# Kernel tuning notes

Measured on AMD Instinct MI355X. Metric: run time of the kernel, lower is better.

## Reference

```python
import jax, jax.numpy as jnp
import numpy as np

INPUT_SCALE = 1.0
TABLE_SIZE = 32
D_EMBED = 64
N = 1_000_000


def setup_inputs() -> dict:
    key = jax.random.key(0)
    k1, k2 = jax.random.split(key)
    x = jax.random.normal(k1, (N, 3), dtype=jnp.float32)
    # learned table parameter: [E, D, H, W] (batch dim of 1 dropped)
    table = jax.random.normal(k2, (D_EMBED, TABLE_SIZE, TABLE_SIZE, TABLE_SIZE), dtype=jnp.float32) * 0.1
    return {"x": x, "table": table}


def _grid_sample_3d(table, grid):
    """F.grid_sample(table[None], grid[None,None,None]) with mode='bilinear',
    padding_mode='zeros', align_corners=False.
    table: [E, D, H, W]; grid: [n, 3] with (x->W, y->H, z->D) order.
    Returns [n, E]."""
    E, Dz, Hy, Wx = table.shape
    sizes_f = jnp.array([Wx, Hy, Dz], dtype=table.dtype)
    dims_i = jnp.array([Wx, Hy, Dz], dtype=jnp.int32)
    # align_corners=False: pix = ((coord + 1) * size - 1) / 2
    pix = ((grid + 1.0) * sizes_f - 1.0) * 0.5   # [n, 3]
    p0f = jnp.floor(pix)
    frac = pix - p0f                              # [n, 3]
    p0 = p0f.astype(jnp.int32)
    tab_flat = table.reshape(E, -1).T             # [D*H*W, E]
    out = jnp.zeros((grid.shape[0], E), dtype=table.dtype)
    for dz in (0, 1):
        for dy in (0, 1):
            for dx in (0, 1):
                off = jnp.array([dx, dy, dz], dtype=jnp.int32)
                idx = p0 + off                                        # [n, 3]
                inb = jnp.all((idx >= 0) & (idx < dims_i), axis=-1)   # zeros padding
                idxc = jnp.clip(idx, 0, dims_i - 1)
                lin = (idxc[:, 2] * Hy + idxc[:, 1]) * Wx + idxc[:, 0]
                vals = tab_flat[lin]                                  # [n, E]
                w = jnp.prod(jnp.where(off == 1, frac, 1.0 - frac), axis=-1)
                out = out + vals * (w * inb.astype(table.dtype))[:, None]
    return out


def reference(x, table):
    xc = jnp.clip(x * INPUT_SCALE, -1.0, 1.0)
    return _grid_sample_3d(table, xc)
```

## Files before the change

### kernel.cpp

```cpp
#include <hip/hip_runtime.h>


constexpr int TSZ = 32;
constexpr int S   = TSZ * TSZ * TSZ;
constexpr int EMB = 64;

__device__ __forceinline__ unsigned short f32_to_bf16_rne(float f) {
  unsigned int u = __float_as_uint(f);
  unsigned int lsb = (u >> 16) & 1u;
  u += 0x7FFFu + lsb;
  return (unsigned short)(u >> 16);
}

__global__ __launch_bounds__(256) void transpose_table_k(
    const float* __restrict__ tab, unsigned short* __restrict__ tabT) {
  __shared__ float tile[EMB][EMB + 1];
  const int s_base = blockIdx.x * 64;
  const int t  = threadIdx.x;
  const int c0 = t & 63;
  const int r0 = t >> 6;
#pragma unroll
  for (int i = 0; i < 16; ++i) {
    const int e = r0 + 4 * i;
    tile[e][c0] = tab[(size_t)e * S + (s_base + c0)];
  }
  __syncthreads();
#pragma unroll
  for (int i = 0; i < 16; ++i) {
    const int s = r0 + 4 * i;
    tabT[(size_t)(s_base + s) * EMB + c0] = f32_to_bf16_rne(tile[c0][s]);
  }
}

__global__ __launch_bounds__(256) void embed_k(
    const float* __restrict__ x, const uint2* __restrict__ tabT,
    float4* __restrict__ out, int n) {
  const int gid = blockIdx.x * 256 + threadIdx.x;
  const int pt  = gid >> 4;
  if (pt >= n) return;
  const int cg = gid & 15;

  const float gx = fminf(fmaxf(x[3 * pt + 0], -1.f), 1.f);
  const float gy = fminf(fmaxf(x[3 * pt + 1], -1.f), 1.f);
  const float gz = fminf(fmaxf(x[3 * pt + 2], -1.f), 1.f);
  const float px = ((gx + 1.f) * 32.f - 1.f) * 0.5f;
  const float py = ((gy + 1.f) * 32.f - 1.f) * 0.5f;
  const float pz = ((gz + 1.f) * 32.f - 1.f) * 0.5f;

  const float fxf = floorf(px), fyf = floorf(py), fzf = floorf(pz);
  const int ix0 = (int)fxf, iy0 = (int)fyf, iz0 = (int)fzf;
  const float fx = px - fxf, fy = py - fyf, fz = pz - fzf;
  const float wx[2] = {1.f - fx, fx};
  const float wy[2] = {1.f - fy, fy};
  const float wz[2] = {1.f - fz, fz};

  float4 acc = make_float4(0.f, 0.f, 0.f, 0.f);
#pragma unroll
  for (int dz = 0; dz < 2; ++dz) {
    const int  iz  = iz0 + dz;
    const bool bz  = (unsigned)iz < (unsigned)TSZ;
    const int  izc = min(max(iz, 0), TSZ - 1);
#pragma unroll
    for (int dy = 0; dy < 2; ++dy) {
      const int  iy  = iy0 + dy;
      const bool by  = (unsigned)iy < (unsigned)TSZ;
      const int  iyc = min(max(iy, 0), TSZ - 1);
#pragma unroll
      for (int dx = 0; dx < 2; ++dx) {
        const int  ix  = ix0 + dx;
        const bool bx  = (unsigned)ix < (unsigned)TSZ;
        const int  ixc = min(max(ix, 0), TSZ - 1);
        float w = wz[dz] * wy[dy] * wx[dx];
        w = (bx && by && bz) ? w : 0.f;
        const int lin = (izc * TSZ + iyc) * TSZ + ixc;
        const uint2 q = tabT[lin * 16 + cg];
        const float v0 = __uint_as_float(q.x << 16);
        const float v1 = __uint_as_float(q.x & 0xFFFF0000u);
        const float v2 = __uint_as_float(q.y << 16);
        const float v3 = __uint_as_float(q.y & 0xFFFF0000u);
        acc.x = fmaf(w, v0, acc.x);
        acc.y = fmaf(w, v1, acc.y);
        acc.z = fmaf(w, v2, acc.z);
        acc.w = fmaf(w, v3, acc.w);
      }
    }
  }
  out[(size_t)pt * (EMB / 4) + cg] = acc;
}

__global__ __launch_bounds__(256) void embed_fallback_k(
    const float* __restrict__ x, const float* __restrict__ tab,
    float* __restrict__ out, int n) {
  const int gid = blockIdx.x * 256 + threadIdx.x;
  const int pt  = gid >> 6;
  if (pt >= n) return;
  const int e = gid & 63;

  const float gx = fminf(fmaxf(x[3 * pt + 0], -1.f), 1.f);
  const float gy = fminf(fmaxf(x[3 * pt + 1], -1.f), 1.f);
  const float gz = fminf(fmaxf(x[3 * pt + 2], -1.f), 1.f);
  const float px = ((gx + 1.f) * 32.f - 1.f) * 0.5f;
  const float py = ((gy + 1.f) * 32.f - 1.f) * 0.5f;
  const float pz = ((gz + 1.f) * 32.f - 1.f) * 0.5f;

  const float fxf = floorf(px), fyf = floorf(py), fzf = floorf(pz);
  const int ix0 = (int)fxf, iy0 = (int)fyf, iz0 = (int)fzf;
  const float fx = px - fxf, fy = py - fyf, fz = pz - fzf;
  const float wx[2] = {1.f - fx, fx};
  const float wy[2] = {1.f - fy, fy};
  const float wz[2] = {1.f - fz, fz};

  float acc = 0.f;
#pragma unroll
  for (int dz = 0; dz < 2; ++dz) {
    const int  iz  = iz0 + dz;
    const bool bz  = (unsigned)iz < (unsigned)TSZ;
    const int  izc = min(max(iz, 0), TSZ - 1);
#pragma unroll
    for (int dy = 0; dy < 2; ++dy) {
      const int  iy  = iy0 + dy;
      const bool by  = (unsigned)iy < (unsigned)TSZ;
      const int  iyc = min(max(iy, 0), TSZ - 1);
#pragma unroll
      for (int dx = 0; dx < 2; ++dx) {
        const int  ix  = ix0 + dx;
        const bool bx  = (unsigned)ix < (unsigned)TSZ;
        const int  ixc = min(max(ix, 0), TSZ - 1);
        float w = wz[dz] * wy[dy] * wx[dx];
        w = (bx && by && bz) ? w : 0.f;
        const int lin = (izc * TSZ + iyc) * TSZ + ixc;
        acc = fmaf(w, tab[(size_t)e * S + lin], acc);
      }
    }
  }
  out[(size_t)pt * EMB + e] = acc;
}

extern "C" void kernel_launch(void* const* d_in, const int* in_sizes, int n_in,
                              void* d_out, int out_size, void* d_ws,
                              size_t ws_size, hipStream_t stream) {
  const float* x   = (const float*)d_in[0];
  const float* tab = (const float*)d_in[1];
  float*       out = (float*)d_out;
  const int n = in_sizes[0] / 3;

  const size_t need = (size_t)S * EMB * sizeof(unsigned short);
  if (ws_size >= need) {
    unsigned short* tabT = (unsigned short*)d_ws;
    transpose_table_k<<<S / 64, 256, 0, stream>>>(tab, tabT);
    const int total  = n * 16;
    const int blocks = (total + 255) / 256;
    embed_k<<<blocks, 256, 0, stream>>>(x, (const uint2*)tabT, (float4*)out, n);
  } else {
    const int total  = n * EMB;
    const int blocks = (total + 255) / 256;
    embed_fallback_k<<<blocks, 256, 0, stream>>>(x, tab, out, n);
  }
}
```

Measured before the change: 331.7 us.

## Widen embed gather to 16-byte loads, 8 channels per thread, nontemporal IO

Result: faster. 319.7 us (-3.6%).

```diff
diff --git a/kernel.cpp b/kernel.cpp
--- a/kernel.cpp
+++ b/kernel.cpp
@@ -4,6 +4,8 @@
 constexpr int TSZ = 32;
 constexpr int S   = TSZ * TSZ * TSZ;
 constexpr int EMB = 64;
+
+typedef float floatx4 __attribute__((ext_vector_type(4)));
 
 __device__ __forceinline__ unsigned short f32_to_bf16_rne(float f) {
   unsigned int u = __float_as_uint(f);
@@ -33,16 +35,16 @@
 }
 
 __global__ __launch_bounds__(256) void embed_k(
-    const float* __restrict__ x, const uint2* __restrict__ tabT,
-    float4* __restrict__ out, int n) {
+    const float* __restrict__ x, const uint4* __restrict__ tabT,
+    float* __restrict__ out, int n) {
   const int gid = blockIdx.x * 256 + threadIdx.x;
-  const int pt  = gid >> 4;
+  const int pt  = gid >> 3;
   if (pt >= n) return;
-  const int cg = gid & 15;
+  const int c8 = gid & 7;
 
-  const float gx = fminf(fmaxf(x[3 * pt + 0], -1.f), 1.f);
-  const float gy = fminf(fmaxf(x[3 * pt + 1], -1.f), 1.f);
-  const float gz = fminf(fmaxf(x[3 * pt + 2], -1.f), 1.f);
+  const float gx = fminf(fmaxf(__builtin_nontemporal_load(&x[3 * pt + 0]), -1.f), 1.f);
+  const float gy = fminf(fmaxf(__builtin_nontemporal_load(&x[3 * pt + 1]), -1.f), 1.f);
+  const float gz = fminf(fmaxf(__builtin_nontemporal_load(&x[3 * pt + 2]), -1.f), 1.f);
   const float px = ((gx + 1.f) * 32.f - 1.f) * 0.5f;
   const float py = ((gy + 1.f) * 32.f - 1.f) * 0.5f;
   const float pz = ((gz + 1.f) * 32.f - 1.f) * 0.5f;
@@ -54,7 +56,10 @@
   const float wy[2] = {1.f - fy, fy};
   const float wz[2] = {1.f - fz, fz};
 
-  float4 acc = make_float4(0.f, 0.f, 0.f, 0.f);
+  float acc[8];
+#pragma unroll
+  for (int k = 0; k < 8; ++k) acc[k] = 0.f;
+
 #pragma unroll
   for (int dz = 0; dz < 2; ++dz) {
     const int  iz  = iz0 + dz;
@@ -65,27 +70,42 @@
       const int  iy  = iy0 + dy;
       const bool by  = (unsigned)iy < (unsigned)TSZ;
       const int  iyc = min(max(iy, 0), TSZ - 1);
+      const int  rowbase = (izc * TSZ + iyc) * TSZ;
+      const float wzy = wz[dz] * wy[dy];
 #pragma unroll
       for (int dx = 0; dx < 2; ++dx) {
         const int  ix  = ix0 + dx;
         const bool bx  = (unsigned)ix < (unsigned)TSZ;
         const int  ixc = min(max(ix, 0), TSZ - 1);
-        float w = wz[dz] * wy[dy] * wx[dx];
+        float w = wzy * wx[dx];
         w = (bx && by && bz) ? w : 0.f;
-        const int lin = (izc * TSZ + iyc) * TSZ + ixc;
-        const uint2 q = tabT[lin * 16 + cg];
+        const int lin = rowbase + ixc;
+        const uint4 q = tabT[lin * 8 + c8];
         const float v0 = __uint_as_float(q.x << 16);
         const float v1 = __uint_as_float(q.x & 0xFFFF0000u);
         const float v2 = __uint_as_float(q.y << 16);
         const float v3 = __uint_as_float(q.y & 0xFFFF0000u);
-        acc.x = fmaf(w, v0, acc.x);
-        acc.y = fmaf(w, v1, acc.y);
-        acc.z = fmaf(w, v2, acc.z);
-        acc.w = fmaf(w, v3, acc.w);
+        const float v4 = __uint_as_float(q.z << 16);
+        const float v5 = __uint_as_float(q.z & 0xFFFF0000u);
+        const float v6 = __uint_as_float(q.w << 16);
+        const float v7 = __uint_as_float(q.w & 0xFFFF0000u);
+        acc[0] = fmaf(w, v0, acc[0]);
+        acc[1] = fmaf(w, v1, acc[1]);
+        acc[2] = fmaf(w, v2, acc[2]);
+        acc[3] = fmaf(w, v3, acc[3]);
+        acc[4] = fmaf(w, v4, acc[4]);
+        acc[5] = fmaf(w, v5, acc[5]);
+        acc[6] = fmaf(w, v6, acc[6]);
+        acc[7] = fmaf(w, v7, acc[7]);
       }
     }
   }
-  out[(size_t)pt * (EMB / 4) + cg] = acc;
+
+  const floatx4 s0 = {acc[0], acc[1], acc[2], acc[3]};
+  const floatx4 s1 = {acc[4], acc[5], acc[6], acc[7]};
+  floatx4* dst = (floatx4*)(out + (size_t)pt * EMB + c8 * 8);
+  __builtin_nontemporal_store(s0, &dst[0]);
+  __builtin_nontemporal_store(s1, &dst[1]);
 }
 
 __global__ __launch_bounds__(256) void embed_fallback_k(
@@ -148,9 +168,9 @@
   if (ws_size >= need) {
     unsigned short* tabT = (unsigned short*)d_ws;
     transpose_table_k<<<S / 64, 256, 0, stream>>>(tab, tabT);
-    const int total  = n * 16;
+    const int total  = n * 8;
     const int blocks = (total + 255) / 256;
-    embed_k<<<blocks, 256, 0, stream>>>(x, (const uint2*)tabT, (float4*)out, n);
+    embed_k<<<blocks, 256, 0, stream>>>(x, (const uint4*)tabT, out, n);
   } else {
     const int total  = n * EMB;
     const int blocks = (total + 255) / 256;
```
